# Optimization experiments

Hardware: AMD Instinct MI355X
Metric: run time of the kernel (lower is better)

The kernel has to match this reference:

```python
import jax, jax.numpy as jnp
import numpy as np

N, C, H, W = 1, 1, 4096, 4096

def setup_inputs() -> dict:
    key = jax.random.key(0)
    x = jax.random.normal(key, (N, C, H, W), dtype=jnp.float32)
    return {"x": x}

def reference(x):
    # torch.median returns the lower of the two middle values for even counts:
    # take the k-th smallest with k = (n-1)//2.
    n = x.size
    median = jnp.sort(x.reshape(-1))[(n - 1) // 2]
    # threshold everything below the median to zero
    thresholded = jnp.where(x < median, jnp.float32(0.0), x)
    # 7x7 max pool, stride 1, padding 3 (torch pads with -inf for max pool)
    pooled = jax.lax.reduce_window(
        thresholded,
        -jnp.inf,
        jax.lax.max,
        window_dimensions=(1, 1, 7, 7),
        window_strides=(1, 1, 1, 1),
        padding=[(0, 0), (0, 0), (3, 3), (3, 3)],
    )
    # In the original, gather(flatten(thresholded), max_indices) == pooled,
    # so binarize where the thresholded value equals its local window max.
    binarized = jnp.where(thresholded == pooled, jnp.float32(1.0), jnp.float32(0.0))
    return binarized * x
```

## Files before the change

kernel.cpp:

```cpp
#include <hip/hip_runtime.h>
#include <math.h>

#define IMG_H 4096
#define IMG_W 4096
#define TS 64
#define HALO 3
#define TW 70
#define THS 71
#define HMS 65
#define NBINS 4096
#define NPACK 2048
#define HBLK 512
#define CAPA 1024
#define CAND_MAX (1u<<22)
#define CB_LO 2047
#define CB_HI 2048
#define RSLOT 32
#define MCAP 1024
#define NSUB 2048

struct SelState {
    unsigned bin;
    unsigned k_rem;
    float    median;
    unsigned flag;
};

__device__ __forceinline__ unsigned f2u(float f) {
    unsigned b = __float_as_uint(f);
    unsigned mask = (unsigned)(-(int)(b >> 31)) | 0x80000000u;
    return b ^ mask;
}
__device__ __forceinline__ float u2f(unsigned u) {
    unsigned mask = (u >> 31) ? 0x80000000u : 0xFFFFFFFFu;
    return __uint_as_float(u ^ mask);
}

__device__ __forceinline__ int val_bin(float v) {
    float t = (v + 4.0f) * 512.0f;
    int b = (int)t;
    b = b < 0 ? 0 : b;
    b = b > (NBINS - 1) ? (NBINS - 1) : b;
    return b;
}

__device__ __forceinline__ int sub_bin(float v) {
    const float lo = (float)(CB_LO - 2048) / 512.0f;
    const float scale = (float)NSUB * 512.0f / (float)(CB_HI + 1 - CB_LO);
    float t = (v - lo) * scale;
    int b = (int)t;
    b = b < 0 ? 0 : b;
    b = b > (NSUB - 1) ? (NSUB - 1) : b;
    return b;
}

__global__ __launch_bounds__(512) void hist_compact(
    const float4* __restrict__ x4, int n4,
    unsigned* __restrict__ gh_priv,
    unsigned* __restrict__ candA, unsigned* __restrict__ cntA)
{
    __shared__ unsigned lh[NPACK];
    __shared__ unsigned buf[CAPA];
    __shared__ unsigned lcnt, gbase;
    const int t = threadIdx.x;
    for (int i = t; i < NPACK; i += 512) lh[i] = 0;
    if (t == 0) lcnt = 0;
    __syncthreads();

    int idx = blockIdx.x * 512 + t;
    int stride = gridDim.x * 512;
    for (int i = idx; i < n4; i += stride) {
        float4 v = x4[i];
        float vs[4] = {v.x, v.y, v.z, v.w};
        #pragma unroll
        for (int j = 0; j < 4; j++) {
            int b = val_bin(vs[j]);
            atomicAdd(&lh[b >> 1], 1u << ((b & 1) * 16));
            if ((unsigned)(b - CB_LO) <= (unsigned)(CB_HI - CB_LO)) {
                unsigned p = atomicAdd(&lcnt, 1u);
                unsigned key = f2u(vs[j]);
                if (p < CAPA) buf[p] = key;
                else {
                    unsigned q = atomicAdd(cntA, 1u);
                    if (q < CAND_MAX) candA[q] = key;
                }
            }
        }
    }
    __syncthreads();
    unsigned* dst = gh_priv + (size_t)blockIdx.x * NPACK;
    for (int i = t; i < NPACK; i += 512) dst[i] = lh[i];
    unsigned m = lcnt; if (m > CAPA) m = CAPA;
    if (t == 0) gbase = atomicAdd(cntA, m);
    __syncthreads();
    for (unsigned i = t; i < m; i += 512) {
        unsigned q = gbase + i;
        if (q < CAND_MAX) candA[q] = buf[i];
    }
}

__global__ __launch_bounds__(256) void reduce_hist(
    const unsigned* __restrict__ gh_priv, unsigned* __restrict__ gh)
{
    const int i = (blockIdx.x & 7) * 256 + threadIdx.x;
    const int r0 = (blockIdx.x >> 3) * 64;
    unsigned lo = 0, hi = 0;
    #pragma unroll 8
    for (int b = 0; b < 64; b++) {
        unsigned d = gh_priv[(size_t)(r0 + b) * NPACK + i];
        lo += d & 0xFFFFu;
        hi += d >> 16;
    }
    atomicAdd(&gh[2 * i],     lo);
    atomicAdd(&gh[2 * i + 1], hi);
}

__global__ __launch_bounds__(1024) void finalize_kernel(
    const unsigned* __restrict__ gh, const unsigned* __restrict__ candA,
    const unsigned* __restrict__ cntA, unsigned K, SelState* __restrict__ st)
{
    __shared__ unsigned hist[NSUB];
    __shared__ unsigned mem[MCAP];
    __shared__ unsigned wsum[16];
    __shared__ unsigned s_bin, s_krem, s_cumlo, s_sb, s_kr2, mcnt;
    const int t = threadIdx.x;
    const unsigned lane = t & 63, wid = t >> 6;

    unsigned cb[4];
    unsigned local = 0;
    #pragma unroll
    for (int j = 0; j < 4; j++) { cb[j] = gh[t * 4 + j]; local += cb[j]; }
    unsigned s = local;
    #pragma unroll
    for (int off = 1; off < 64; off <<= 1) {
        unsigned u = __shfl_up(s, off, 64);
        if (lane >= off) s += u;
    }
    if (lane == 63) wsum[wid] = s;
    if (t == 0) mcnt = 0;
    __syncthreads();
    unsigned base = 0;
    for (unsigned w = 0; w < wid; w++) base += wsum[w];
    unsigned excl = base + s - local;
    if (K >= excl && K < excl + local) {
        unsigned cum = excl;
        #pragma unroll
        for (int j = 0; j < 4; j++) {
            if (K < cum + cb[j]) { s_bin = (unsigned)(t * 4 + j); s_krem = K - cum; break; }
            cum += cb[j];
        }
    }
    if (t == (CB_LO >> 2)) {
        unsigned c = excl;
        #pragma unroll
        for (int j = 0; j < 4; j++) if (((CB_LO >> 2) * 4 + j) < CB_LO) c += cb[j];
        s_cumlo = c;
    }
    __syncthreads();

    const unsigned bsel = s_bin;
    const unsigned M = *cntA;
    const bool direct = (bsel >= CB_LO) && (bsel <= CB_HI) && (M <= RSLOT * 1024u);

    if (!direct) {
        if (t == 0) { st->bin = bsel; st->k_rem = s_krem; st->flag = 0; }
        return;
    }

    const unsigned kRem = K - s_cumlo;

    unsigned rc[RSLOT];
    #pragma unroll
    for (int j = 0; j < RSLOT; j++) {
        int i = j * 1024 + t;
        rc[j] = (i < (int)M) ? candA[i] : 0u;
    }
    for (int i = t; i < NSUB; i += 1024) hist[i] = 0;
    __syncthreads();

    #pragma unroll
    for (int j = 0; j < RSLOT; j++) {
        int i = j * 1024 + t;
        if (i < (int)M) atomicAdd(&hist[sub_bin(u2f(rc[j]))], 1u);
    }
    __syncthreads();

    unsigned d0 = hist[t * 2], d1 = hist[t * 2 + 1];
    unsigned loc2 = d0 + d1;
    unsigned s2 = loc2;
    #pragma unroll
    for (int off = 1; off < 64; off <<= 1) {
        unsigned u = __shfl_up(s2, off, 64);
        if (lane >= off) s2 += u;
    }
    if (lane == 63) wsum[wid] = s2;
    __syncthreads();
    unsigned base2 = 0;
    for (unsigned w = 0; w < wid; w++) base2 += wsum[w];
    unsigned excl2 = base2 + s2 - loc2;
    if (kRem >= excl2 && kRem < excl2 + loc2) {
        if (kRem < excl2 + d0) { s_sb = (unsigned)(t * 2);     s_kr2 = kRem - excl2; }
        else                   { s_sb = (unsigned)(t * 2 + 1); s_kr2 = kRem - excl2 - d0; }
    }
    __syncthreads();

    const int sb = (int)s_sb;
    #pragma unroll
    for (int j = 0; j < RSLOT; j++) {
        int i = j * 1024 + t;
        if (i < (int)M && sub_bin(u2f(rc[j])) == sb) {
            unsigned p = atomicAdd(&mcnt, 1u);
            if (p < MCAP) mem[p] = rc[j];
        }
    }
    __syncthreads();

    if (mcnt > MCAP) {
        if (t == 0) { st->bin = bsel; st->k_rem = s_krem; st->flag = 0; }
        return;
    }

    const unsigned m = mcnt;
    const unsigned kr2 = s_kr2;
    if ((unsigned)t < m) {
        unsigned ku = mem[t];
        unsigned c = 0, e = 0;
        for (unsigned j = 0; j < m; j++) {
            unsigned kj = mem[j];
            c += (kj < ku);
            e += (kj == ku);
        }
        if (c <= kr2 && kr2 < c + e) { st->median = u2f(ku); st->flag = 1; }
    }
}

__device__ unsigned radix_select_256(const unsigned* __restrict__ cand, int M,
                                     unsigned kRem0)
{
    __shared__ unsigned hist[2048];
    __shared__ unsigned wsum[4];
    __shared__ unsigned s_pref, s_krem;
    const int t = threadIdx.x;
    if (t == 0) { s_pref = 0; s_krem = kRem0; }

    for (int p = 0; p < 3; p++) {
        const int shift = (p == 0) ? 21 : ((p == 1) ? 10 : 0);
        const int bits  = (p == 2) ? 10 : 11;
        const int nb    = 1 << bits;
        for (int i = t; i < nb; i += 256) hist[i] = 0;
        __syncthreads();
        const unsigned pref = s_pref;
        for (int i = t; i < M; i += 256) {
            unsigned u = cand[i];
            bool ok = (p == 0) || ((u >> ((p == 1) ? 21 : 10)) == pref);
            if (ok) atomicAdd(&hist[(u >> shift) & (unsigned)(nb - 1)], 1u);
        }
        __syncthreads();
        const int P = nb >> 8;
        unsigned cb[8];
        unsigned local = 0;
        for (int j = 0; j < P; j++) { cb[j] = hist[t * P + j]; local += cb[j]; }
        const unsigned lane = t & 63, wid = t >> 6;
        unsigned s = local;
        #pragma unroll
        for (int off = 1; off < 64; off <<= 1) {
            unsigned u = __shfl_up(s, off, 64);
            if (lane >= off) s += u;
        }
        if (lane == 63) wsum[wid] = s;
        __syncthreads();
        unsigned base = 0;
        for (unsigned w = 0; w < wid; w++) base += wsum[w];
        unsigned excl = base + s - local;
        unsigned kRem = s_krem;
        __syncthreads();
        if (kRem >= excl && kRem < excl + local) {
            unsigned cum = excl;
            for (int j = 0; j < P; j++) {
                if (kRem < cum + cb[j]) {
                    s_pref = (pref << bits) | (unsigned)(t * P + j);
                    s_krem = kRem - cum;
                    break;
                }
                cum += cb[j];
            }
        }
        __syncthreads();
    }
    return s_pref;
}

__global__ __launch_bounds__(256) void fallback_compact(
    const float4* __restrict__ x4, int n4, const SelState* __restrict__ st,
    unsigned* __restrict__ candB, unsigned* __restrict__ cntB)
{
    if (st->flag) return;
    __shared__ unsigned buf[CAPA];
    __shared__ unsigned lcnt, gbase;
    const int t = threadIdx.x;
    if (t == 0) lcnt = 0;
    __syncthreads();
    const int b = (int)st->bin;
    int idx = blockIdx.x * 256 + t;
    int stride = gridDim.x * 256;
    for (int i = idx; i < n4; i += stride) {
        float4 v = x4[i];
        float vs[4] = {v.x, v.y, v.z, v.w};
        #pragma unroll
        for (int j = 0; j < 4; j++) {
            if (val_bin(vs[j]) == b) {
                unsigned p = atomicAdd(&lcnt, 1u);
                if (p < CAPA) buf[p] = f2u(vs[j]);
                else { unsigned q = atomicAdd(cntB, 1u); candB[q] = f2u(vs[j]); }
            }
        }
    }
    __syncthreads();
    unsigned m = lcnt; if (m > CAPA) m = CAPA;
    if (t == 0) gbase = atomicAdd(cntB, m);
    __syncthreads();
    for (unsigned i = t; i < m; i += 256) candB[gbase + i] = buf[i];
}

__global__ __launch_bounds__(256) void fallback_select(
    const unsigned* __restrict__ candB, const unsigned* __restrict__ cntB,
    SelState* __restrict__ st)
{
    if (st->flag) return;
    unsigned key = radix_select_256(candB, (int)*cntB, st->k_rem);
    if (threadIdx.x == 0) st->median = u2f(key);
}

__global__ __launch_bounds__(512) void nms_kernel(
    const float* __restrict__ x, float* __restrict__ out,
    const SelState* __restrict__ st)
{
    __shared__ float th[TW * THS];
    __shared__ float hm[TW * HMS];

    const float med = st->median;
    const float NEGINF = -__builtin_inff();
    const int gx0 = blockIdx.x * TS - HALO;
    const int gy0 = blockIdx.y * TS - HALO;

    for (int i = threadIdx.x; i < TW * TW; i += 512) {
        int r = i / TW, c = i - r * TW;
        int gy = gy0 + r, gx = gx0 + c;
        float v = NEGINF;
        if (gy >= 0 && gy < IMG_H && gx >= 0 && gx < IMG_W) {
            v = x[gy * IMG_W + gx];
            v = (v < med) ? 0.0f : v;
        }
        th[r * THS + c] = v;
    }
    __syncthreads();

    for (int task = threadIdx.x; task < TW * 8; task += 512) {
        int r = task % TW;
        int c0 = (task / TW) * 8;
        float w[7];
        #pragma unroll
        for (int i = 0; i < 14; i++) {
            w[i % 7] = th[r * THS + c0 + i];
            if (i >= 6) {
                float m = w[0];
                #pragma unroll
                for (int k = 1; k < 7; k++) m = fmaxf(m, w[k]);
                hm[r * HMS + c0 + i - 6] = m;
            }
        }
    }
    __syncthreads();

    {
        const int c = threadIdx.x & 63;
        const int rr0 = (threadIdx.x >> 6) * 8;
        float w[7];
        #pragma unroll
        for (int i = 0; i < 14; i++) {
            w[i % 7] = hm[(rr0 + i) * HMS + c];
            if (i >= 6) {
                int R = rr0 + i - 6;
                float m = w[0];
                #pragma unroll
                for (int k = 1; k < 7; k++) m = fmaxf(m, w[k]);
                float t = th[(R + HALO) * THS + (c + HALO)];
                int gy = blockIdx.y * TS + R;
                int gx = blockIdx.x * TS + c;
                float o = 0.0f;
                if (t == m) {
                    o = (t != 0.0f) ? t : x[gy * IMG_W + gx];
                }
                out[gy * IMG_W + gx] = o;
            }
        }
    }
}

extern "C" void kernel_launch(void* const* d_in, const int* in_sizes, int n_in,
                              void* d_out, int out_size, void* d_ws, size_t ws_size,
                              hipStream_t stream)
{
    const float* x = (const float*)d_in[0];
    float* out = (float*)d_out;
    const int n = in_sizes[0];
    const unsigned K = (unsigned)((n - 1) / 2);

    char* ws = (char*)d_ws;
    unsigned* gh      = (unsigned*)ws;
    unsigned* cntA    = (unsigned*)(ws + 16384);
    unsigned* cntB    = (unsigned*)(ws + 16388);
    SelState* st      = (SelState*)(ws + 16400);
    unsigned* gh_priv = (unsigned*)(ws + ws_size / 4);
    unsigned* candA   = (unsigned*)(ws + ws_size / 2);

    hipMemsetAsync(d_ws, 0, 16416, stream);

    const int n4 = n / 4;
    hist_compact<<<HBLK, 512, 0, stream>>>((const float4*)x, n4, gh_priv, candA, cntA);
    reduce_hist<<<64, 256, 0, stream>>>(gh_priv, gh);
    finalize_kernel<<<1, 1024, 0, stream>>>(gh, candA, cntA, K, st);
    fallback_compact<<<512, 256, 0, stream>>>((const float4*)x, n4, st,
                                              (unsigned*)d_out, cntB);
    fallback_select<<<1, 256, 0, stream>>>((const unsigned*)d_out, cntB, st);

    dim3 fg(IMG_W / TS, IMG_H / TS);
    nms_kernel<<<fg, 512, 0, stream>>>(x, out, st);
}
```

Baseline: 158.5 us.

## Replace full histogram with below-count plus window compaction for median select

The first pass no longer builds a 4096-bin shared histogram per block. It only counts elements below a narrow window around zero and compacts the in-window values, which drops the per-element LDS histogram atomics and the separate histogram-reduce kernel. The full histogram is moved into a fallback path that runs only when the median falls outside the window. The NMS tile load is also rewritten to use float4 global loads. The fast path assumes the median lies near zero, but a correct fallback is kept.

Measured after the change: 150.7 us. 1.05x faster.

```diff
diff --git a/kernel.cpp b/kernel.cpp
--- a/kernel.cpp
+++ b/kernel.cpp
@@ -9,12 +9,11 @@
 #define THS 71
 #define HMS 65
 #define NBINS 4096
-#define NPACK 2048
-#define HBLK 512
-#define CAPA 1024
+#define CBLK 512
+#define CAPA 2048
 #define CAND_MAX (1u<<22)
-#define CB_LO 2047
-#define CB_HI 2048
+#define WLO (-0.001953125f)
+#define WHI ( 0.001953125f)
 #define RSLOT 32
 #define MCAP 1024
 #define NSUB 2048
@@ -45,28 +44,26 @@
 }
 
 __device__ __forceinline__ int sub_bin(float v) {
-    const float lo = (float)(CB_LO - 2048) / 512.0f;
-    const float scale = (float)NSUB * 512.0f / (float)(CB_HI + 1 - CB_LO);
-    float t = (v - lo) * scale;
+    float t = (v - WLO) * (float)(NSUB * 256);
     int b = (int)t;
     b = b < 0 ? 0 : b;
     b = b > (NSUB - 1) ? (NSUB - 1) : b;
     return b;
 }
 
-__global__ __launch_bounds__(512) void hist_compact(
+__global__ __launch_bounds__(512) void count_compact(
     const float4* __restrict__ x4, int n4,
-    unsigned* __restrict__ gh_priv,
+    unsigned* __restrict__ belowArr,
     unsigned* __restrict__ candA, unsigned* __restrict__ cntA)
 {
-    __shared__ unsigned lh[NPACK];
     __shared__ unsigned buf[CAPA];
+    __shared__ unsigned wred[8];
     __shared__ unsigned lcnt, gbase;
     const int t = threadIdx.x;
-    for (int i = t; i < NPACK; i += 512) lh[i] = 0;
     if (t == 0) lcnt = 0;
     __syncthreads();
 
+    unsigned below = 0;
     int idx = blockIdx.x * 512 + t;
     int stride = gridDim.x * 512;
     for (int i = idx; i < n4; i += stride) {
@@ -74,100 +71,67 @@
         float vs[4] = {v.x, v.y, v.z, v.w};
         #pragma unroll
         for (int j = 0; j < 4; j++) {
-            int b = val_bin(vs[j]);
-            atomicAdd(&lh[b >> 1], 1u << ((b & 1) * 16));
-            if ((unsigned)(b - CB_LO) <= (unsigned)(CB_HI - CB_LO)) {
+            float vv = vs[j];
+            below += (vv < WLO) ? 1u : 0u;
+            if (vv >= WLO && vv < WHI) {
                 unsigned p = atomicAdd(&lcnt, 1u);
-                unsigned key = f2u(vs[j]);
+                unsigned key = f2u(vv);
                 if (p < CAPA) buf[p] = key;
-                else {
-                    unsigned q = atomicAdd(cntA, 1u);
-                    if (q < CAND_MAX) candA[q] = key;
-                }
-            }
-        }
-    }
-    __syncthreads();
-    unsigned* dst = gh_priv + (size_t)blockIdx.x * NPACK;
-    for (int i = t; i < NPACK; i += 512) dst[i] = lh[i];
+                else { unsigned q = atomicAdd(cntA, 1u); if (q < CAND_MAX) candA[q] = key; }
+            }
+        }
+    }
+    #pragma unroll
+    for (int off = 32; off >= 1; off >>= 1) below += __shfl_down(below, off, 64);
+    if ((t & 63) == 0) wred[t >> 6] = below;
+    __syncthreads();
+    if (t == 0) {
+        unsigned tot = 0;
+        #pragma unroll
+        for (int w = 0; w < 8; w++) tot += wred[w];
+        belowArr[blockIdx.x] = tot;
+        gbase = atomicAdd(cntA, (lcnt > CAPA) ? CAPA : lcnt);
+    }
+    __syncthreads();
     unsigned m = lcnt; if (m > CAPA) m = CAPA;
-    if (t == 0) gbase = atomicAdd(cntA, m);
-    __syncthreads();
     for (unsigned i = t; i < m; i += 512) {
         unsigned q = gbase + i;
         if (q < CAND_MAX) candA[q] = buf[i];
     }
 }
 
-__global__ __launch_bounds__(256) void reduce_hist(
-    const unsigned* __restrict__ gh_priv, unsigned* __restrict__ gh)
-{
-    const int i = (blockIdx.x & 7) * 256 + threadIdx.x;
-    const int r0 = (blockIdx.x >> 3) * 64;
-    unsigned lo = 0, hi = 0;
-    #pragma unroll 8
-    for (int b = 0; b < 64; b++) {
-        unsigned d = gh_priv[(size_t)(r0 + b) * NPACK + i];
-        lo += d & 0xFFFFu;
-        hi += d >> 16;
-    }
-    atomicAdd(&gh[2 * i],     lo);
-    atomicAdd(&gh[2 * i + 1], hi);
-}
-
 __global__ __launch_bounds__(1024) void finalize_kernel(
-    const unsigned* __restrict__ gh, const unsigned* __restrict__ candA,
-    const unsigned* __restrict__ cntA, unsigned K, SelState* __restrict__ st)
+    const unsigned* __restrict__ belowArr,
+    const unsigned* __restrict__ candA, const unsigned* __restrict__ cntA,
+    unsigned K, SelState* __restrict__ st)
 {
     __shared__ unsigned hist[NSUB];
     __shared__ unsigned mem[MCAP];
     __shared__ unsigned wsum[16];
-    __shared__ unsigned s_bin, s_krem, s_cumlo, s_sb, s_kr2, mcnt;
+    __shared__ unsigned s_below, s_sb, s_kr2, mcnt;
     const int t = threadIdx.x;
     const unsigned lane = t & 63, wid = t >> 6;
 
-    unsigned cb[4];
-    unsigned local = 0;
-    #pragma unroll
-    for (int j = 0; j < 4; j++) { cb[j] = gh[t * 4 + j]; local += cb[j]; }
-    unsigned s = local;
-    #pragma unroll
-    for (int off = 1; off < 64; off <<= 1) {
-        unsigned u = __shfl_up(s, off, 64);
-        if (lane >= off) s += u;
-    }
-    if (lane == 63) wsum[wid] = s;
+    unsigned b = (t < CBLK) ? belowArr[t] : 0u;
+    #pragma unroll
+    for (int off = 32; off >= 1; off >>= 1) b += __shfl_down(b, off, 64);
+    if (lane == 0) wsum[wid] = b;
     if (t == 0) mcnt = 0;
     __syncthreads();
-    unsigned base = 0;
-    for (unsigned w = 0; w < wid; w++) base += wsum[w];
-    unsigned excl = base + s - local;
-    if (K >= excl && K < excl + local) {
-        unsigned cum = excl;
-        #pragma unroll
-        for (int j = 0; j < 4; j++) {
-            if (K < cum + cb[j]) { s_bin = (unsigned)(t * 4 + j); s_krem = K - cum; break; }
-            cum += cb[j];
-        }
-    }
-    if (t == (CB_LO >> 2)) {
-        unsigned c = excl;
-        #pragma unroll
-        for (int j = 0; j < 4; j++) if (((CB_LO >> 2) * 4 + j) < CB_LO) c += cb[j];
-        s_cumlo = c;
-    }
-    __syncthreads();
-
-    const unsigned bsel = s_bin;
+    if (t == 0) {
+        unsigned tot = 0;
+        #pragma unroll
+        for (int w = 0; w < 16; w++) tot += wsum[w];
+        s_below = tot;
+    }
+    __syncthreads();
+
+    const unsigned below = s_below;
     const unsigned M = *cntA;
-    const bool direct = (bsel >= CB_LO) && (bsel <= CB_HI) && (M <= RSLOT * 1024u);
-
-    if (!direct) {
-        if (t == 0) { st->bin = bsel; st->k_rem = s_krem; st->flag = 0; }
-        return;
-    }
-
-    const unsigned kRem = K - s_cumlo;
+    const bool direct = (K >= below) && (K - below < M) && (M <= RSLOT * 1024u);
+    if (!direct) return;
+
+    const unsigned kRem = K - below;
 
     unsigned rc[RSLOT];
     #pragma unroll
@@ -214,11 +178,7 @@
         }
     }
     __syncthreads();
-
-    if (mcnt > MCAP) {
-        if (t == 0) { st->bin = bsel; st->k_rem = s_krem; st->flag = 0; }
-        return;
-    }
+    if (mcnt > MCAP) return;
 
     const unsigned m = mcnt;
     const unsigned kr2 = s_kr2;
@@ -234,14 +194,109 @@
     }
 }
 
-__device__ unsigned radix_select_256(const unsigned* __restrict__ cand, int M,
-                                     unsigned kRem0)
-{
+
+__global__ __launch_bounds__(256) void fb_hist(
+    const float4* __restrict__ x4, int n4, const SelState* __restrict__ st,
+    unsigned* __restrict__ gh)
+{
+    if (st->flag) return;
+    __shared__ unsigned lh[NBINS];
+    for (int i = threadIdx.x; i < NBINS; i += 256) lh[i] = 0;
+    __syncthreads();
+    int idx = blockIdx.x * 256 + threadIdx.x;
+    int stride = gridDim.x * 256;
+    for (int i = idx; i < n4; i += stride) {
+        float4 v = x4[i];
+        atomicAdd(&lh[val_bin(v.x)], 1u);
+        atomicAdd(&lh[val_bin(v.y)], 1u);
+        atomicAdd(&lh[val_bin(v.z)], 1u);
+        atomicAdd(&lh[val_bin(v.w)], 1u);
+    }
+    __syncthreads();
+    for (int i = threadIdx.x; i < NBINS; i += 256) {
+        unsigned c = lh[i];
+        if (c) atomicAdd(&gh[i], c);
+    }
+}
+
+__global__ __launch_bounds__(1024) void fb_scan(
+    const unsigned* __restrict__ gh, unsigned K, SelState* __restrict__ st)
+{
+    if (st->flag) return;
+    __shared__ unsigned wsum[16];
+    __shared__ unsigned s_bin, s_krem;
+    const int t = threadIdx.x;
+    const unsigned lane = t & 63, wid = t >> 6;
+    unsigned cb[4];
+    unsigned local = 0;
+    #pragma unroll
+    for (int j = 0; j < 4; j++) { cb[j] = gh[t * 4 + j]; local += cb[j]; }
+    unsigned s = local;
+    #pragma unroll
+    for (int off = 1; off < 64; off <<= 1) {
+        unsigned u = __shfl_up(s, off, 64);
+        if (lane >= off) s += u;
+    }
+    if (lane == 63) wsum[wid] = s;
+    __syncthreads();
+    unsigned base = 0;
+    for (unsigned w = 0; w < wid; w++) base += wsum[w];
+    unsigned excl = base + s - local;
+    if (K >= excl && K < excl + local) {
+        unsigned cum = excl;
+        #pragma unroll
+        for (int j = 0; j < 4; j++) {
+            if (K < cum + cb[j]) { s_bin = (unsigned)(t * 4 + j); s_krem = K - cum; break; }
+            cum += cb[j];
+        }
+    }
+    __syncthreads();
+    if (t == 0) { st->bin = s_bin; st->k_rem = s_krem; }
+}
+
+__global__ __launch_bounds__(256) void fb_compact(
+    const float4* __restrict__ x4, int n4, const SelState* __restrict__ st,
+    unsigned* __restrict__ candB, unsigned* __restrict__ cntB)
+{
+    if (st->flag) return;
+    __shared__ unsigned buf[CAPA];
+    __shared__ unsigned lcnt, gbase;
+    const int t = threadIdx.x;
+    if (t == 0) lcnt = 0;
+    __syncthreads();
+    const int b = (int)st->bin;
+    int idx = blockIdx.x * 256 + t;
+    int stride = gridDim.x * 256;
+    for (int i = idx; i < n4; i += stride) {
+        float4 v = x4[i];
+        float vs[4] = {v.x, v.y, v.z, v.w};
+        #pragma unroll
+        for (int j = 0; j < 4; j++) {
+            if (val_bin(vs[j]) == b) {
+                unsigned p = atomicAdd(&lcnt, 1u);
+                if (p < CAPA) buf[p] = f2u(vs[j]);
+                else { unsigned q = atomicAdd(cntB, 1u); candB[q] = f2u(vs[j]); }
+            }
+        }
+    }
+    __syncthreads();
+    unsigned m = lcnt; if (m > CAPA) m = CAPA;
+    if (t == 0) gbase = atomicAdd(cntB, m);
+    __syncthreads();
+    for (unsigned i = t; i < m; i += 256) candB[gbase + i] = buf[i];
+}
+
+__global__ __launch_bounds__(256) void fb_select(
+    const unsigned* __restrict__ candB, const unsigned* __restrict__ cntB,
+    SelState* __restrict__ st)
+{
+    if (st->flag) return;
     __shared__ unsigned hist[2048];
     __shared__ unsigned wsum[4];
     __shared__ unsigned s_pref, s_krem;
     const int t = threadIdx.x;
-    if (t == 0) { s_pref = 0; s_krem = kRem0; }
+    const int M = (int)*cntB;
+    if (t == 0) { s_pref = 0; s_krem = st->k_rem; }
 
     for (int p = 0; p < 3; p++) {
         const int shift = (p == 0) ? 21 : ((p == 1) ? 10 : 0);
@@ -251,7 +306,7 @@
         __syncthreads();
         const unsigned pref = s_pref;
         for (int i = t; i < M; i += 256) {
-            unsigned u = cand[i];
+            unsigned u = candB[i];
             bool ok = (p == 0) || ((u >> ((p == 1) ? 21 : 10)) == pref);
             if (ok) atomicAdd(&hist[(u >> shift) & (unsigned)(nb - 1)], 1u);
         }
@@ -287,48 +342,7 @@
         }
         __syncthreads();
     }
-    return s_pref;
-}
-
-__global__ __launch_bounds__(256) void fallback_compact(
-    const float4* __restrict__ x4, int n4, const SelState* __restrict__ st,
-    unsigned* __restrict__ candB, unsigned* __restrict__ cntB)
-{
-    if (st->flag) return;
-    __shared__ unsigned buf[CAPA];
-    __shared__ unsigned lcnt, gbase;
-    const int t = threadIdx.x;
-    if (t == 0) lcnt = 0;
-    __syncthreads();
-    const int b = (int)st->bin;
-    int idx = blockIdx.x * 256 + t;
-    int stride = gridDim.x * 256;
-    for (int i = idx; i < n4; i += stride) {
-        float4 v = x4[i];
-        float vs[4] = {v.x, v.y, v.z, v.w};
-        #pragma unroll
-        for (int j = 0; j < 4; j++) {
-            if (val_bin(vs[j]) == b) {
-                unsigned p = atomicAdd(&lcnt, 1u);
-                if (p < CAPA) buf[p] = f2u(vs[j]);
-                else { unsigned q = atomicAdd(cntB, 1u); candB[q] = f2u(vs[j]); }
-            }
-        }
-    }
-    __syncthreads();
-    unsigned m = lcnt; if (m > CAPA) m = CAPA;
-    if (t == 0) gbase = atomicAdd(cntB, m);
-    __syncthreads();
-    for (unsigned i = t; i < m; i += 256) candB[gbase + i] = buf[i];
-}
-
-__global__ __launch_bounds__(256) void fallback_select(
-    const unsigned* __restrict__ candB, const unsigned* __restrict__ cntB,
-    SelState* __restrict__ st)
-{
-    if (st->flag) return;
-    unsigned key = radix_select_256(candB, (int)*cntB, st->k_rem);
-    if (threadIdx.x == 0) st->median = u2f(key);
+    if (t == 0) st->median = u2f(s_pref);
 }
 
 __global__ __launch_bounds__(512) void nms_kernel(
@@ -340,18 +354,37 @@
 
     const float med = st->median;
     const float NEGINF = -__builtin_inff();
-    const int gx0 = blockIdx.x * TS - HALO;
-    const int gy0 = blockIdx.y * TS - HALO;
-
-    for (int i = threadIdx.x; i < TW * TW; i += 512) {
-        int r = i / TW, c = i - r * TW;
-        int gy = gy0 + r, gx = gx0 + c;
-        float v = NEGINF;
-        if (gy >= 0 && gy < IMG_H && gx >= 0 && gx < IMG_W) {
-            v = x[gy * IMG_W + gx];
-            v = (v < med) ? 0.0f : v;
-        }
-        th[r * THS + c] = v;
+    const int bx = blockIdx.x, by = blockIdx.y;
+    const int gy0 = by * TS - HALO;
+    const int gcol0 = bx * TS - 4;
+
+    for (int task = threadIdx.x; task < TW * 18; task += 512) {
+        int r = task / 18, q = task - r * 18;
+        int gy = gy0 + r;
+        int gxb = gcol0 + q * 4;
+        bool rowok = (gy >= 0 && gy < IMG_H);
+        float vs[4];
+        if (rowok && gxb >= 0 && gxb + 4 <= IMG_W) {
+            float4 v = *(const float4*)&x[gy * IMG_W + gxb];
+            vs[0] = v.x; vs[1] = v.y; vs[2] = v.z; vs[3] = v.w;
+        } else if (rowok) {
+            #pragma unroll
+            for (int cmp = 0; cmp < 4; cmp++) {
+                int gx = gxb + cmp;
+                vs[cmp] = (gx >= 0 && gx < IMG_W) ? x[gy * IMG_W + gx] : NEGINF;
+            }
+        } else {
+            vs[0] = vs[1] = vs[2] = vs[3] = NEGINF;
+        }
+        #pragma unroll
+        for (int cmp = 0; cmp < 4; cmp++) {
+            int c = q * 4 - 1 + cmp;
+            if ((unsigned)c < (unsigned)TW) {
+                float v = vs[cmp];
+                v = (v == NEGINF) ? v : ((v < med) ? 0.0f : v);
+                th[r * THS + c] = v;
+            }
+        }
     }
     __syncthreads();
 
@@ -385,8 +418,8 @@
                 #pragma unroll
                 for (int k = 1; k < 7; k++) m = fmaxf(m, w[k]);
                 float t = th[(R + HALO) * THS + (c + HALO)];
-                int gy = blockIdx.y * TS + R;
-                int gx = blockIdx.x * TS + c;
+                int gy = by * TS + R;
+                int gx = bx * TS + c;
                 float o = 0.0f;
                 if (t == m) {
                     o = (t != 0.0f) ? t : x[gy * IMG_W + gx];
@@ -407,22 +440,22 @@
     const unsigned K = (unsigned)((n - 1) / 2);
 
     char* ws = (char*)d_ws;
-    unsigned* gh      = (unsigned*)ws;
-    unsigned* cntA    = (unsigned*)(ws + 16384);
-    unsigned* cntB    = (unsigned*)(ws + 16388);
-    SelState* st      = (SelState*)(ws + 16400);
-    unsigned* gh_priv = (unsigned*)(ws + ws_size / 4);
-    unsigned* candA   = (unsigned*)(ws + ws_size / 2);
+    unsigned* gh       = (unsigned*)ws;
+    unsigned* cntA     = (unsigned*)(ws + 16384);
+    unsigned* cntB     = (unsigned*)(ws + 16388);
+    SelState* st       = (SelState*)(ws + 16400);
+    unsigned* belowArr = (unsigned*)(ws + 16640);
+    unsigned* candA    = (unsigned*)(ws + ws_size / 2);
 
     hipMemsetAsync(d_ws, 0, 16416, stream);
 
     const int n4 = n / 4;
-    hist_compact<<<HBLK, 512, 0, stream>>>((const float4*)x, n4, gh_priv, candA, cntA);
-    reduce_hist<<<64, 256, 0, stream>>>(gh_priv, gh);
-    finalize_kernel<<<1, 1024, 0, stream>>>(gh, candA, cntA, K, st);
-    fallback_compact<<<512, 256, 0, stream>>>((const float4*)x, n4, st,
-                                              (unsigned*)d_out, cntB);
-    fallback_select<<<1, 256, 0, stream>>>((const unsigned*)d_out, cntB, st);
+    count_compact<<<CBLK, 512, 0, stream>>>((const float4*)x, n4, belowArr, candA, cntA);
+    finalize_kernel<<<1, 1024, 0, stream>>>(belowArr, candA, cntA, K, st);
+    fb_hist<<<512, 256, 0, stream>>>((const float4*)x, n4, st, gh);
+    fb_scan<<<1, 1024, 0, stream>>>(gh, K, st);
+    fb_compact<<<512, 256, 0, stream>>>((const float4*)x, n4, st, (unsigned*)d_out, cntB);
+    fb_select<<<1, 256, 0, stream>>>((const unsigned*)d_out, cntB, st);
 
     dim3 fg(IMG_W / TS, IMG_H / TS);
     nms_kernel<<<fg, 512, 0, stream>>>(x, out, st);
```
